# Kernel tuning notes

Measured on AMD Instinct MI355X. Metric: run time of the kernel, lower is better.

Reference implementation:

```python
import jax, jax.numpy as jnp
import numpy as np

VOCAB = 50257
DIM = 768
B, S = 2, 2048
SINKHORN_ITERS = 5
SINKHORN_EPS = 0.05


def setup_inputs() -> dict:
    key = jax.random.key(0)
    k1, k2 = jax.random.split(key)
    x = jax.random.normal(k1, (B, S, DIM), dtype=jnp.float32)
    vocab_weight = jax.random.normal(k2, (VOCAB, DIM), dtype=jnp.float32)
    bias = jnp.zeros((VOCAB,), dtype=jnp.float32)
    return {"x": x, "vocab_weight": vocab_weight, "bias": bias}


def _l2norm(v, axis=-1, eps=1e-12):
    # matches F.normalize: v / max(||v||, eps)
    n = jnp.sqrt(jnp.sum(v * v, axis=axis, keepdims=True))
    return v / jnp.maximum(n, eps)


def reference(x, vocab_weight, bias):
    x_norm = _l2norm(x)                      # [B, S, D]
    w_norm = _l2norm(vocab_weight)           # [V, D]
    logits = jnp.einsum('bsd,vd->bsv', x_norm, w_norm)  # cosine sims [B, S, V]
    eps = max(float(SINKHORN_EPS), 1e-6)
    logits = logits / eps
    for _ in range(SINKHORN_ITERS):
        # logits - logsumexp(logits, -1) == log_softmax (stable, single pass)
        logits = jax.nn.log_softmax(logits, axis=-1)
    return logits + bias
```

## Files before the change

kernel.cpp:

```cpp
#include <hip/hip_runtime.h>
#include <cstdint>
#include <cstddef>

#define VOCAB  50257
#define VPAD   50304
#define DIMK   768
#define MROWS  4096
#define NBLK   393
#define MBLK   32
#define LSCALE 20.0f

typedef __bf16 bf16x8 __attribute__((ext_vector_type(8)));
typedef float  floatx4 __attribute__((ext_vector_type(4)));

typedef const void __attribute__((address_space(1)))* gptr1_t;
typedef void __attribute__((address_space(3)))* lptr3_t;

__device__ __forceinline__ void async_copy16(const void* g, void* l) {
  __builtin_amdgcn_global_load_lds((gptr1_t)g, (lptr3_t)l, 16, 0, 0);
}

__device__ __forceinline__ unsigned short f2bf(float f) {
  union { float f; unsigned u; } x; x.f = f;
  unsigned r = x.u + 0x7fffu + ((x.u >> 16) & 1u);
  return (unsigned short)(r >> 16);
}

__global__ void norm_rows_kernel(const float* __restrict__ in,
                                 unsigned short* __restrict__ outb,
                                 int valid_rows) {
  const int row = blockIdx.x;
  const int t = threadIdx.x;
  float v0 = 0.f, v1 = 0.f, v2 = 0.f;
  if (row < valid_rows) {
    const float* p = in + (size_t)row * DIMK;
    v0 = p[t]; v1 = p[t + 256]; v2 = p[t + 512];
  }
  float ss = v0 * v0 + v1 * v1 + v2 * v2;
#pragma unroll
  for (int off = 32; off > 0; off >>= 1) ss += __shfl_xor(ss, off);
  __shared__ float wss[4];
  if ((t & 63) == 0) wss[t >> 6] = ss;
  __syncthreads();
  const float tot = wss[0] + wss[1] + wss[2] + wss[3];
  const float sc = 1.0f / fmaxf(sqrtf(tot), 1e-12f);
  unsigned short* q = outb + (size_t)row * DIMK;
  q[t]       = f2bf(v0 * sc);
  q[t + 256] = f2bf(v1 * sc);
  q[t + 512] = f2bf(v2 * sc);
}

__global__ __launch_bounds__(256)
void gemm_kernel(const unsigned short* __restrict__ A,
                 const unsigned short* __restrict__ Bw,
                 float* __restrict__ out,
                 float* __restrict__ row_sums) {
  __shared__ __align__(16) unsigned short As[128 * 32];
  __shared__ __align__(16) unsigned short Bs[128 * 32];
  const int tid  = threadIdx.x;
  const int wave = tid >> 6;
  const int lane = tid & 63;
  const int lhi  = lane >> 4;
  const int llo  = lane & 15;
  const int wm   = wave >> 1;
  const int wn   = wave & 1;
  const int rowBase = blockIdx.y * 128;
  const int colBase = blockIdx.x * 128;

  floatx4 acc[4][4];
#pragma unroll
  for (int i = 0; i < 4; ++i)
#pragma unroll
    for (int j = 0; j < 4; ++j)
      acc[i][j] = (floatx4){0.f, 0.f, 0.f, 0.f};

  const int c0 = (wave * 2 + 0) * 64 + lane;
  const int c1 = (wave * 2 + 1) * 64 + lane;
  const unsigned short* Ag0 = A  + (size_t)(rowBase + (c0 >> 2)) * DIMK + (c0 & 3) * 8;
  const unsigned short* Ag1 = A  + (size_t)(rowBase + (c1 >> 2)) * DIMK + (c1 & 3) * 8;
  const unsigned short* Bg0 = Bw + (size_t)(colBase + (c0 >> 2)) * DIMK + (c0 & 3) * 8;
  const unsigned short* Bg1 = Bw + (size_t)(colBase + (c1 >> 2)) * DIMK + (c1 & 3) * 8;
  unsigned short* Al0 = As + (wave * 2 + 0) * 512;
  unsigned short* Al1 = As + (wave * 2 + 1) * 512;
  unsigned short* Bl0 = Bs + (wave * 2 + 0) * 512;
  unsigned short* Bl1 = Bs + (wave * 2 + 1) * 512;

  for (int k0 = 0; k0 < DIMK; k0 += 32) {
    __syncthreads();
    async_copy16(Ag0 + k0, Al0);
    async_copy16(Ag1 + k0, Al1);
    async_copy16(Bg0 + k0, Bl0);
    async_copy16(Bg1 + k0, Bl1);
    __syncthreads();

    bf16x8 af[4], bfr[4];
#pragma unroll
    for (int fr = 0; fr < 4; ++fr)
      af[fr] = *(const bf16x8*)&As[(wm * 64 + fr * 16 + llo) * 32 + lhi * 8];
#pragma unroll
    for (int fc = 0; fc < 4; ++fc)
      bfr[fc] = *(const bf16x8*)&Bs[(wn * 64 + fc * 16 + llo) * 32 + lhi * 8];
#pragma unroll
    for (int fr = 0; fr < 4; ++fr)
#pragma unroll
      for (int fc = 0; fc < 4; ++fc)
        acc[fr][fc] = __builtin_amdgcn_mfma_f32_16x16x32_bf16(
            af[fr], bfr[fc], acc[fr][fc], 0, 0, 0);
  }

  const int growBase = rowBase + wm * 64;
  const int gcolBase = colBase + wn * 64;
  float myrowsum = 0.f;
  int   myrow = growBase;
#pragma unroll
  for (int fr = 0; fr < 4; ++fr) {
#pragma unroll
    for (int r = 0; r < 4; ++r) {
      const int grow = growBase + fr * 16 + lhi * 4 + r;
      float s = 0.f;
#pragma unroll
      for (int fc = 0; fc < 4; ++fc) {
        const int gcol = gcolBase + fc * 16 + llo;
        const float l = acc[fr][fc][r] * LSCALE;
        if (gcol < VOCAB) {
          out[(size_t)grow * VOCAB + gcol] = l;
          s += __expf(l - LSCALE);
        }
      }
      s += __shfl_xor(s, 1);
      s += __shfl_xor(s, 2);
      s += __shfl_xor(s, 4);
      s += __shfl_xor(s, 8);
      if (llo == fr * 4 + r) { myrowsum = s; myrow = grow; }
    }
  }
  atomicAdd(&row_sums[myrow], myrowsum);
}

__global__ void lse_fin_kernel(const float* __restrict__ sums,
                               float* __restrict__ lse) {
  const int i = blockIdx.x * 256 + threadIdx.x;
  if (i < MROWS) lse[i] = LSCALE + logf(sums[i]);
}

#define TOT4 51463168u
__global__ void apply_kernel(float* __restrict__ out,
                             const float* __restrict__ lse,
                             const float* __restrict__ bias) {
  const unsigned i = blockIdx.x * 256 + threadIdx.x;
  if (i >= TOT4) return;
  float4 v = reinterpret_cast<float4*>(out)[i];
  const unsigned b0 = i * 4u;
  unsigned idx, row, col;
  idx = b0 + 0u; row = idx / (unsigned)VOCAB; col = idx - row * (unsigned)VOCAB;
  v.x = v.x - lse[row] + bias[col];
  idx = b0 + 1u; row = idx / (unsigned)VOCAB; col = idx - row * (unsigned)VOCAB;
  v.y = v.y - lse[row] + bias[col];
  idx = b0 + 2u; row = idx / (unsigned)VOCAB; col = idx - row * (unsigned)VOCAB;
  v.z = v.z - lse[row] + bias[col];
  idx = b0 + 3u; row = idx / (unsigned)VOCAB; col = idx - row * (unsigned)VOCAB;
  v.w = v.w - lse[row] + bias[col];
  reinterpret_cast<float4*>(out)[i] = v;
}

extern "C" void kernel_launch(void* const* d_in, const int* in_sizes, int n_in,
                              void* d_out, int out_size, void* d_ws, size_t ws_size,
                              hipStream_t stream) {
  const float* x    = (const float*)d_in[0];
  const float* w    = (const float*)d_in[1];
  const float* bias = (const float*)d_in[2];
  float* out = (float*)d_out;

  unsigned short* xn = (unsigned short*)d_ws;
  unsigned short* wn = xn + (size_t)MROWS * DIMK;
  float* sums = (float*)(wn + (size_t)VPAD * DIMK);
  float* lse  = sums + MROWS;

  hipMemsetAsync(sums, 0, MROWS * sizeof(float), stream);
  norm_rows_kernel<<<MROWS, 256, 0, stream>>>(x, xn, MROWS);
  norm_rows_kernel<<<VPAD, 256, 0, stream>>>(w, wn, VOCAB);
  dim3 g(NBLK, MBLK);
  gemm_kernel<<<g, 256, 0, stream>>>(xn, wn, out, sums);
  lse_fin_kernel<<<(MROWS + 255) / 256, 256, 0, stream>>>(sums, lse);
  apply_kernel<<<(TOT4 + 255u) / 256u, 256, 0, stream>>>(out, lse, bias);
}
```

Measured before the change: 1.712 ms.

## Double-buffer GEMM LDS, swizzle tiles, use nontemporal stores, grid-stride apply kernel

The GEMM now double-buffers its LDS tiles so the next K slice loads while MFMAs run, and XOR-swizzles the LDS layout to avoid bank conflicts. It also remaps block IDs so consecutive workgroups are spread across row tiles, and uses nontemporal stores for the logits. The apply kernel becomes grid-stride, does one division per float4 instead of four, and uses nontemporal loads and stores. Together these target LDS latency and stalls, bank conflicts, cache pollution and integer-divide overhead, at the cost of twice the LDS per block.

```diff
diff --git a/kernel.cpp b/kernel.cpp
--- a/kernel.cpp
+++ b/kernel.cpp
@@ -8,6 +8,8 @@
 #define MROWS  4096
 #define NBLK   393
 #define MBLK   32
+#define NWG    (NBLK * MBLK)
+#define KSTEPS (DIMK / 32)
 #define LSCALE 20.0f
 
 typedef __bf16 bf16x8 __attribute__((ext_vector_type(8)));
@@ -55,8 +57,8 @@
                  const unsigned short* __restrict__ Bw,
                  float* __restrict__ out,
                  float* __restrict__ row_sums) {
-  __shared__ __align__(16) unsigned short As[128 * 32];
-  __shared__ __align__(16) unsigned short Bs[128 * 32];
+  __shared__ __align__(16) unsigned short As[2][128 * 32];
+  __shared__ __align__(16) unsigned short Bs[2][128 * 32];
   const int tid  = threadIdx.x;
   const int wave = tid >> 6;
   const int lane = tid & 63;
@@ -64,8 +66,13 @@
   const int llo  = lane & 15;
   const int wm   = wave >> 1;
   const int wn   = wave & 1;
-  const int rowBase = blockIdx.y * 128;
-  const int colBase = blockIdx.x * 128;
+
+  const int orig = (int)blockIdx.x;
+  const int swz  = (orig & 7) * (NWG / 8) + (orig >> 3);
+  const int by   = swz / NBLK;
+  const int bx   = swz - by * NBLK;
+  const int rowBase = by * 128;
+  const int colBase = bx * 128;
 
   floatx4 acc[4][4];
 #pragma unroll
@@ -76,55 +83,77 @@
 
   const int c0 = (wave * 2 + 0) * 64 + lane;
   const int c1 = (wave * 2 + 1) * 64 + lane;
-  const unsigned short* Ag0 = A  + (size_t)(rowBase + (c0 >> 2)) * DIMK + (c0 & 3) * 8;
-  const unsigned short* Ag1 = A  + (size_t)(rowBase + (c1 >> 2)) * DIMK + (c1 & 3) * 8;
-  const unsigned short* Bg0 = Bw + (size_t)(colBase + (c0 >> 2)) * DIMK + (c0 & 3) * 8;
-  const unsigned short* Bg1 = Bw + (size_t)(colBase + (c1 >> 2)) * DIMK + (c1 & 3) * 8;
-  unsigned short* Al0 = As + (wave * 2 + 0) * 512;
-  unsigned short* Al1 = As + (wave * 2 + 1) * 512;
-  unsigned short* Bl0 = Bs + (wave * 2 + 0) * 512;
-  unsigned short* Bl1 = Bs + (wave * 2 + 1) * 512;
-
-  for (int k0 = 0; k0 < DIMK; k0 += 32) {
-    __syncthreads();
-    async_copy16(Ag0 + k0, Al0);
-    async_copy16(Ag1 + k0, Al1);
-    async_copy16(Bg0 + k0, Bl0);
-    async_copy16(Bg1 + k0, Bl1);
-    __syncthreads();
-
+  const int r0 = c0 >> 2, r1 = c1 >> 2;
+  const int q0 = (c0 & 3) ^ ((r0 >> 1) & 3);
+  const int q1 = (c1 & 3) ^ ((r1 >> 1) & 3);
+  const unsigned short* Ag0 = A  + (size_t)(rowBase + r0) * DIMK + q0 * 8;
+  const unsigned short* Ag1 = A  + (size_t)(rowBase + r1) * DIMK + q1 * 8;
+  const unsigned short* Bg0 = Bw + (size_t)(colBase + r0) * DIMK + q0 * 8;
+  const unsigned short* Bg1 = Bw + (size_t)(colBase + r1) * DIMK + q1 * 8;
+  const int l0 = (wave * 2 + 0) * 512;
+  const int l1 = (wave * 2 + 1) * 512;
+
+  async_copy16(Ag0, &As[0][l0]);
+  async_copy16(Ag1, &As[0][l1]);
+  async_copy16(Bg0, &Bs[0][l0]);
+  async_copy16(Bg1, &Bs[0][l1]);
+  __syncthreads();
+
+  const int kcS = (lhi ^ ((llo >> 1) & 3)) * 8;
+
+  int cur = 0;
+  for (int kt = 0; kt < KSTEPS; ++kt) {
+    if (kt + 1 < KSTEPS) {
+      const int kn = (kt + 1) * 32;
+      const int nb = cur ^ 1;
+      async_copy16(Ag0 + kn, &As[nb][l0]);
+      async_copy16(Ag1 + kn, &As[nb][l1]);
+      async_copy16(Bg0 + kn, &Bs[nb][l0]);
+      async_copy16(Bg1 + kn, &Bs[nb][l1]);
+    }
     bf16x8 af[4], bfr[4];
 #pragma unroll
     for (int fr = 0; fr < 4; ++fr)
-      af[fr] = *(const bf16x8*)&As[(wm * 64 + fr * 16 + llo) * 32 + lhi * 8];
+      af[fr] = *(const bf16x8*)&As[cur][(wm * 64 + fr * 16 + llo) * 32 + kcS];
 #pragma unroll
     for (int fc = 0; fc < 4; ++fc)
-      bfr[fc] = *(const bf16x8*)&Bs[(wn * 64 + fc * 16 + llo) * 32 + lhi * 8];
+      bfr[fc] = *(const bf16x8*)&Bs[cur][(wn * 64 + fc * 16 + llo) * 32 + kcS];
 #pragma unroll
     for (int fr = 0; fr < 4; ++fr)
 #pragma unroll
       for (int fc = 0; fc < 4; ++fc)
         acc[fr][fc] = __builtin_amdgcn_mfma_f32_16x16x32_bf16(
             af[fr], bfr[fc], acc[fr][fc], 0, 0, 0);
-  }
-
-  const int growBase = rowBase + wm * 64;
-  const int gcolBase = colBase + wn * 64;
+    __syncthreads();
+    cur ^= 1;
+  }
+
+  const bool tail = (colBase + 128 > VOCAB);
   float myrowsum = 0.f;
-  int   myrow = growBase;
+  int   myrow = rowBase + wm * 64;
 #pragma unroll
   for (int fr = 0; fr < 4; ++fr) {
 #pragma unroll
     for (int r = 0; r < 4; ++r) {
-      const int grow = growBase + fr * 16 + lhi * 4 + r;
+      const int grow = rowBase + wm * 64 + fr * 16 + lhi * 4 + r;
+      float* orow = out + (size_t)grow * VOCAB + colBase + wn * 64;
       float s = 0.f;
-#pragma unroll
-      for (int fc = 0; fc < 4; ++fc) {
-        const int gcol = gcolBase + fc * 16 + llo;
-        const float l = acc[fr][fc][r] * LSCALE;
-        if (gcol < VOCAB) {
-          out[(size_t)grow * VOCAB + gcol] = l;
+      if (!tail) {
+#pragma unroll
+        for (int fc = 0; fc < 4; ++fc) {
+          const float l = acc[fr][fc][r] * LSCALE;
+          __builtin_nontemporal_store(l, &orow[fc * 16 + llo]);
           s += __expf(l - LSCALE);
+        }
+      } else {
+#pragma unroll
+        for (int fc = 0; fc < 4; ++fc) {
+          const int gcol = colBase + wn * 64 + fc * 16 + llo;
+          if (gcol < VOCAB) {
+            const float l = acc[fr][fc][r] * LSCALE;
+            __builtin_nontemporal_store(l, &orow[fc * 16 + llo]);
+            s += __expf(l - LSCALE);
+          }
         }
       }
       s += __shfl_xor(s, 1);
@@ -144,23 +173,26 @@
 }
 
 #define TOT4 51463168u
-__global__ void apply_kernel(float* __restrict__ out,
-                             const float* __restrict__ lse,
-                             const float* __restrict__ bias) {
-  const unsigned i = blockIdx.x * 256 + threadIdx.x;
-  if (i >= TOT4) return;
-  float4 v = reinterpret_cast<float4*>(out)[i];
-  const unsigned b0 = i * 4u;
-  unsigned idx, row, col;
-  idx = b0 + 0u; row = idx / (unsigned)VOCAB; col = idx - row * (unsigned)VOCAB;
-  v.x = v.x - lse[row] + bias[col];
-  idx = b0 + 1u; row = idx / (unsigned)VOCAB; col = idx - row * (unsigned)VOCAB;
-  v.y = v.y - lse[row] + bias[col];
-  idx = b0 + 2u; row = idx / (unsigned)VOCAB; col = idx - row * (unsigned)VOCAB;
-  v.z = v.z - lse[row] + bias[col];
-  idx = b0 + 3u; row = idx / (unsigned)VOCAB; col = idx - row * (unsigned)VOCAB;
-  v.w = v.w - lse[row] + bias[col];
-  reinterpret_cast<float4*>(out)[i] = v;
+__global__ __launch_bounds__(256)
+void apply_kernel(float* __restrict__ out,
+                  const float* __restrict__ lse,
+                  const float* __restrict__ bias) {
+  const unsigned stride = gridDim.x * 256u;
+  floatx4* o4 = reinterpret_cast<floatx4*>(out);
+  for (unsigned i = blockIdx.x * 256u + threadIdx.x; i < TOT4; i += stride) {
+    floatx4 v = __builtin_nontemporal_load(o4 + i);
+    const unsigned b0 = i * 4u;
+    unsigned row = b0 / (unsigned)VOCAB;
+    unsigned col = b0 - row * (unsigned)VOCAB;
+    float lr = lse[row];
+#pragma unroll
+    for (int j = 0; j < 4; ++j) {
+      if (col == (unsigned)VOCAB) { col = 0u; ++row; lr = lse[row]; }
+      v[j] = v[j] - lr + bias[col];
+      ++col;
+    }
+    __builtin_nontemporal_store(v, o4 + i);
+  }
 }
 
 extern "C" void kernel_launch(void* const* d_in, const int* in_sizes, int n_in,
@@ -179,8 +211,7 @@
   hipMemsetAsync(sums, 0, MROWS * sizeof(float), stream);
   norm_rows_kernel<<<MROWS, 256, 0, stream>>>(x, xn, MROWS);
   norm_rows_kernel<<<VPAD, 256, 0, stream>>>(w, wn, VOCAB);
-  dim3 g(NBLK, MBLK);
-  gemm_kernel<<<g, 256, 0, stream>>>(xn, wn, out, sums);
+  gemm_kernel<<<NWG, 256, 0, stream>>>(xn, wn, out, sums);
   lse_fin_kernel<<<(MROWS + 255) / 256, 256, 0, stream>>>(sums, lse);
-  apply_kernel<<<(TOT4 + 255u) / 256u, 256, 0, stream>>>(out, lse, bias);
-}
+  apply_kernel<<<4096, 256, 0, stream>>>(out, lse, bias);
+}
```

Result: slower. 1.826 ms (+6.7%).
